# Kernel optimization log

Hardware: AMD Instinct MI355X
Metric: run time of the kernel (lower is better)

## Reference

```python
import jax, jax.numpy as jnp
import numpy as np

N = 3072      # nodes
D = 256       # embed_dim
H = 8         # heads
E = 98304     # edges (avg degree 32)
B = 16        # graphs in batch


def setup_inputs() -> dict:
    key = jax.random.key(0)
    ks = jax.random.split(key, 14)
    w = lambda k, sh: jax.random.normal(k, sh, jnp.float32) * 0.02
    return {
        "x": jax.random.normal(ks[0], (N, D), jnp.float32),
        "edge_attr": jax.random.normal(ks[1], (E, 4), jnp.float32),
        "Wq": w(ks[2], (D, D)), "bq": jnp.zeros((D,), jnp.float32),
        "Wk": w(ks[3], (D, D)), "bk": jnp.zeros((D,), jnp.float32),
        "Wv": w(ks[4], (D, D)), "bv": jnp.zeros((D,), jnp.float32),
        "Wo": w(ks[5], (D, D)), "bo": jnp.zeros((D,), jnp.float32),
        "We": w(ks[6], (4, H)), "be": jnp.zeros((H,), jnp.float32),
        "edge_index": jax.random.randint(ks[7], (2, E), 0, N),
        "batch": jnp.sort(jax.random.randint(ks[8], (N,), 0, B)),
    }


def reference(x, edge_attr, Wq, bq, Wk, bk, Wv, bv, Wo, bo, We, be,
              edge_index, batch):
    n, d = x.shape
    h = be.shape[0]
    hd = d // h
    # projections -> [h, n, hd]
    Q = (x @ Wq + bq).reshape(n, h, hd).transpose(1, 0, 2)
    K = (x @ Wk + bk).reshape(n, h, hd).transpose(1, 0, 2)
    V = (x @ Wv + bv).reshape(n, h, hd).transpose(1, 0, 2)
    # dense attention scores [h, n, n]
    scores = jnp.einsum('hnd,hmd->hnm', Q, K) / np.float32(np.sqrt(hd))
    # per-edge bias scatter-add (accumulate over duplicate edges)
    edge_bias = edge_attr @ We + be                     # [E, h]
    scores = scores.at[:, edge_index[0], edge_index[1]].add(edge_bias.T)
    # block-diagonal batch mask
    same_graph = batch[:, None] == batch[None, :]       # [n, n]
    scores = jnp.where(same_graph[None], scores, -jnp.inf)
    attn = jax.nn.softmax(scores, axis=-1)              # dropout: eval mode (identity)
    out = jnp.einsum('hnm,hmd->hnd', attn, V)           # [h, n, hd]
    out = out.transpose(1, 0, 2).reshape(n, d)
    return out @ Wo + bo
```

## Files before the change

### kernel.cpp

```cpp
#include <hip/hip_runtime.h>
#include <hip/hip_bf16.h>
#include <math.h>

#define N_NODES 3072
#define DIM     256
#define NH      8
#define HD      32
#define E_EDGES 98304
#define B_GRAPHS 16
#define MAXC    390
#define PADP    392
#define TR      16
#define SCALE   0.17677669529663689f

typedef __attribute__((ext_vector_type(8))) short bf16x8;
typedef __attribute__((ext_vector_type(4))) float f32x4;
typedef __attribute__((ext_vector_type(4))) unsigned short ushort4v;

__device__ inline unsigned short f2b(float f) {
    __hip_bfloat16 h = __float2bfloat16(f);
    return *reinterpret_cast<unsigned short*>(&h);
}
__device__ inline float b2f(unsigned short u) {
    __hip_bfloat16 h = *reinterpret_cast<__hip_bfloat16*>(&u);
    return __bfloat162float(h);
}

__global__ __launch_bounds__(256) void prep(
    const float* __restrict__ x,
    const float* __restrict__ Wq, const float* __restrict__ Wk,
    const float* __restrict__ Wv, const float* __restrict__ Wo,
    unsigned short* __restrict__ xh, unsigned short* __restrict__ xl,
    unsigned short* __restrict__ Wth, unsigned short* __restrict__ Wtl,
    const int* __restrict__ batch, int* __restrict__ counts, int* __restrict__ gstart)
{
    const int b = blockIdx.x, t = threadIdx.x;
    if (b < 768) {
        const int gid = b * 256 + t;
        float4 v = ((const float4*)x)[gid];
        ushort4v h, l;
        float c[4] = {v.x, v.y, v.z, v.w};
        #pragma unroll
        for (int i = 0; i < 4; ++i) {
            unsigned short hi = f2b(c[i]);
            h[i] = hi;
            l[i] = f2b(c[i] - b2f(hi));
        }
        ((ushort4v*)xh)[gid] = h;
        ((ushort4v*)xl)[gid] = l;
    } else if (b < 1024) {
        __shared__ float tile[32][33];
        const int wb = b - 768;
        const int mat = wb >> 6, tidx = wb & 63;
        const int tk = (tidx >> 3) * 32, tn = (tidx & 7) * 32;
        const float* W = (mat == 0) ? Wq : (mat == 1) ? Wk : (mat == 2) ? Wv : Wo;
        const int kk = t >> 5, nn = t & 31;
        #pragma unroll
        for (int p = 0; p < 4; ++p)
            tile[nn][kk + p * 8] = W[(size_t)(tk + kk + p * 8) * DIM + tn + nn];
        __syncthreads();
        const int n = t >> 3, kq = (t & 7) * 4;
        ushort4v h, l;
        #pragma unroll
        for (int i = 0; i < 4; ++i) {
            float v = tile[n][kq + i];
            unsigned short hi = f2b(v);
            h[i] = hi;
            l[i] = f2b(v - b2f(hi));
        }
        size_t o = (size_t)mat * DIM * DIM + (size_t)(tn + n) * DIM + tk + kq;
        *(ushort4v*)(Wth + o) = h;
        *(ushort4v*)(Wtl + o) = l;
    } else {
        const int i = (b - 1024) * 256 + t;
        if (i < 2 * N_NODES) counts[i] = 0;
        if (i < N_NODES) {
            int bb = batch[i];
            int bp = (i == 0) ? -1 : batch[i - 1];
            for (int g = bp + 1; g <= bb; ++g) gstart[g] = i;
            if (i == N_NODES - 1)
                for (int g = bb + 1; g <= B_GRAPHS; ++g) gstart[g] = N_NODES;
        }
    }
}

__global__ __launch_bounds__(256) void qkv_mfma(
    const unsigned short* __restrict__ xh, const unsigned short* __restrict__ xl,
    const unsigned short* __restrict__ Wth, const unsigned short* __restrict__ Wtl,
    const float* __restrict__ bq, const float* __restrict__ bk, const float* __restrict__ bv,
    unsigned short* __restrict__ Qb, unsigned short* __restrict__ Kb,
    unsigned short* __restrict__ Vb)
{
    const int t = threadIdx.x, w = t >> 6, lane = t & 63;
    const int l16 = lane & 15, lq = lane >> 4;
    const int mat = blockIdx.y >> 1;
    const int rb = blockIdx.x * 32 + (w & 1) * 16;
    const int nb = (blockIdx.y & 1) * 128 + (w >> 1) * 64;
    const unsigned short* Wh = Wth + (size_t)mat * DIM * DIM;
    const unsigned short* Wl = Wtl + (size_t)mat * DIM * DIM;

    f32x4 acc[4] = {{0,0,0,0},{0,0,0,0},{0,0,0,0},{0,0,0,0}};
    const size_t arow = (size_t)(rb + l16) * DIM + (lq << 3);

    #pragma unroll
    for (int kc = 0; kc < 8; ++kc) {
        const int k = kc * 32;
        bf16x8 ah = *(const bf16x8*)(xh + arow + k);
        bf16x8 al = *(const bf16x8*)(xl + arow + k);
        #pragma unroll
        for (int ct = 0; ct < 4; ++ct) {
            const size_t bo_ = (size_t)(nb + ct * 16 + l16) * DIM + k + (lq << 3);
            bf16x8 bh = *(const bf16x8*)(Wh + bo_);
            bf16x8 bl = *(const bf16x8*)(Wl + bo_);
            acc[ct] = __builtin_amdgcn_mfma_f32_16x16x32_bf16(ah, bh, acc[ct], 0, 0, 0);
            acc[ct] = __builtin_amdgcn_mfma_f32_16x16x32_bf16(ah, bl, acc[ct], 0, 0, 0);
            acc[ct] = __builtin_amdgcn_mfma_f32_16x16x32_bf16(al, bh, acc[ct], 0, 0, 0);
        }
    }

    const float* bias = (mat == 0) ? bq : (mat == 1) ? bk : bv;
    unsigned short* outp = (mat == 0) ? Qb : (mat == 1) ? Kb : Vb;
    #pragma unroll
    for (int ct = 0; ct < 4; ++ct) {
        const int n = nb + ct * 16 + l16;
        const float bvl = bias[n];
        #pragma unroll
        for (int r = 0; r < 4; ++r) {
            const int row = rb + lq * 4 + r;
            outp[(size_t)row * DIM + n] = f2b(acc[ct][r] + bvl);
        }
    }
}

__global__ void edge_count(const int* __restrict__ erow, int* __restrict__ counts) {
    int e = blockIdx.x * blockDim.x + threadIdx.x;
    if (e < E_EDGES) atomicAdd(&counts[erow[e]], 1);
}

__global__ __launch_bounds__(1024) void scan_rows(const int* __restrict__ counts,
                                                  int* __restrict__ rowstart) {
    __shared__ int lds[1024];
    const int t = threadIdx.x;
    int c0 = counts[3 * t], c1 = counts[3 * t + 1], c2 = counts[3 * t + 2];
    int local = c0 + c1 + c2;
    lds[t] = local;
    __syncthreads();
    for (int off = 1; off < 1024; off <<= 1) {
        int v = (t >= off) ? lds[t - off] : 0;
        __syncthreads();
        lds[t] += v;
        __syncthreads();
    }
    int incl = lds[t];
    int base = incl - local;
    rowstart[3 * t]     = base;
    rowstart[3 * t + 1] = base + c0;
    rowstart[3 * t + 2] = base + c0 + c1;
    if (t == 1023) rowstart[N_NODES] = incl;
}

__global__ void edge_fill(const int* __restrict__ erow, const int* __restrict__ ecolin,
                          const float* __restrict__ ea, const float* __restrict__ We,
                          const float* __restrict__ be,
                          const int* __restrict__ rowstart, int* __restrict__ cursor,
                          int* __restrict__ ecol, float* __restrict__ ebias) {
    int e = blockIdx.x * blockDim.x + threadIdx.x;
    if (e >= E_EDGES) return;
    int row = erow[e];
    int pos = rowstart[row] + atomicAdd(&cursor[row], 1);
    ecol[pos] = ecolin[e];
    float a0 = ea[e * 4 + 0], a1 = ea[e * 4 + 1], a2 = ea[e * 4 + 2], a3 = ea[e * 4 + 3];
    #pragma unroll
    for (int h = 0; h < NH; ++h) {
        float b = fmaf(a0, We[0 * NH + h],
                  fmaf(a1, We[1 * NH + h],
                  fmaf(a2, We[2 * NH + h],
                  fmaf(a3, We[3 * NH + h], be[h]))));
        ebias[(size_t)h * E_EDGES + pos] = b;
    }
}

__global__ __launch_bounds__(256) void attn(
    const unsigned short* __restrict__ Qb, const unsigned short* __restrict__ Kb,
    const unsigned short* __restrict__ Vb,
    const int* __restrict__ gstart, const int* __restrict__ rowstart,
    const int* __restrict__ ecol, const float* __restrict__ ebias,
    unsigned short* __restrict__ preh, unsigned short* __restrict__ prel)
{
    __shared__ float s[TR][MAXC];
    __shared__ unsigned short pb[TR][PADP];
    __shared__ float rowinv[TR];
    __shared__ int   rs_sh[TR + 1];

    const int g = blockIdx.x, tile = blockIdx.y, h = blockIdx.z;
    const int gs = gstart[g], ge = gstart[g + 1];
    const int row0 = gs + tile * TR;
    if (row0 >= ge) return;
    const int nrows = min(TR, ge - row0);
    const int ncols = ge - gs;
    const int cpad  = (ncols + 31) & ~31;
    const int t = threadIdx.x;
    const int wave = t >> 6, lane = t & 63;
    const int l16 = lane & 15, lq = lane >> 4;

    if (t <= nrows) rs_sh[t] = rowstart[row0 + t];

    {
        int arow = min(row0 + l16, N_NODES - 1);
        const bf16x8 aq = *(const bf16x8*)(Qb + (size_t)arow * DIM + h * HD + (lq << 3));
        const int nchunk16 = (ncols + 15) >> 4;
        for (int j = wave; j < nchunk16; j += 4) {
            const int c0 = j << 4;
            int krow = min(gs + c0 + l16, N_NODES - 1);
            bf16x8 bk = *(const bf16x8*)(Kb + (size_t)krow * DIM + h * HD + (lq << 3));
            f32x4 d = {0.f, 0.f, 0.f, 0.f};
            d = __builtin_amdgcn_mfma_f32_16x16x32_bf16(aq, bk, d, 0, 0, 0);
            const int col = c0 + l16, rbase = lq * 4;
            #pragma unroll
            for (int r = 0; r < 4; ++r) s[rbase + r][col] = d[r] * SCALE;
        }
    }
    __syncthreads();

    {
        int e0 = rs_sh[0], e1 = rs_sh[nrows];
        for (int idx = e0 + t; idx < e1; idx += 256) {
            int lo = 0, hi = nrows;
            while (hi - lo > 1) {
                int mid = (lo + hi) >> 1;
                if (rs_sh[mid] <= idx) lo = mid; else hi = mid;
            }
            int col = ecol[idx] - gs;
            if (col >= 0 && col < ncols)
                atomicAdd(&s[lo][col], ebias[(size_t)h * E_EDGES + idx]);
        }
    }
    __syncthreads();

    {
        const int r = t >> 4, sub = t & 15;
        if (r < nrows) {
            float m = -INFINITY;
            for (int c = sub; c < ncols; c += 16) m = fmaxf(m, s[r][c]);
            m = fmaxf(m, __shfl_xor(m, 1, 16));
            m = fmaxf(m, __shfl_xor(m, 2, 16));
            m = fmaxf(m, __shfl_xor(m, 4, 16));
            m = fmaxf(m, __shfl_xor(m, 8, 16));
            float sum = 0.f;
            for (int c = sub; c < cpad; c += 16) {
                if (c < ncols) {
                    float e = __expf(s[r][c] - m);
                    sum += e;
                    pb[r][c] = f2b(e);
                } else {
                    pb[r][c] = 0;
                }
            }
            sum += __shfl_xor(sum, 1, 16);
            sum += __shfl_xor(sum, 2, 16);
            sum += __shfl_xor(sum, 4, 16);
            sum += __shfl_xor(sum, 8, 16);
            if (sub == 0) rowinv[r] = 1.0f / sum;
        } else {
            for (int c = sub; c < cpad; c += 16) pb[r][c] = 0;
        }
    }
    __syncthreads();

    f32x4 o = {0.f, 0.f, 0.f, 0.f};
    {
        const int half = wave >> 1, par = wave & 1;
        const int kout = l16 + (half << 4);
        const int nchunk32 = cpad >> 5;
        for (int j = par; j < nchunk32; j += 2) {
            const int c0 = j << 5;
            bf16x8 ap = *(const bf16x8*)(&pb[l16][c0 + (lq << 3)]);
            bf16x8 bv;
            const int cb = c0 + (lq << 3);
            #pragma unroll
            for (int jj = 0; jj < 8; ++jj) {
                int vr = min(gs + cb + jj, N_NODES - 1);
                bv[jj] = (short)Vb[(size_t)vr * DIM + h * HD + kout];
            }
            o = __builtin_amdgcn_mfma_f32_16x16x32_bf16(ap, bv, o, 0, 0, 0);
        }
    }
    __syncthreads();
    {
        float* red = &s[0][0];
        const int rbase = lq * 4;
        #pragma unroll
        for (int r = 0; r < 4; ++r)
            red[((wave << 4) + rbase + r) * 17 + l16] = o[r];
    }
    __syncthreads();
    {
        const int row = t >> 4, kl = t & 15;
        if (row < nrows) {
            float* red = &s[0][0];
            float v0 = red[(row) * 17 + kl]        + red[(16 + row) * 17 + kl];
            float v1 = red[(32 + row) * 17 + kl]   + red[(48 + row) * 17 + kl];
            float sc = rowinv[row];
            size_t ob = (size_t)(row0 + row) * DIM + h * HD;
            float f0 = v0 * sc, f1 = v1 * sc;
            unsigned short h0 = f2b(f0), h1 = f2b(f1);
            preh[ob + kl]      = h0;
            preh[ob + 16 + kl] = h1;
            prel[ob + kl]      = f2b(f0 - b2f(h0));
            prel[ob + 16 + kl] = f2b(f1 - b2f(h1));
        }
    }
}

__global__ __launch_bounds__(256) void out_mfma(
    const unsigned short* __restrict__ preh, const unsigned short* __restrict__ prel,
    const unsigned short* __restrict__ Wth, const unsigned short* __restrict__ Wtl,
    const float* __restrict__ bo, float* __restrict__ out)
{
    const int t = threadIdx.x, w = t >> 6, lane = t & 63;
    const int l16 = lane & 15, lq = lane >> 4;
    const int rb = blockIdx.x * 16;
    const int nb = blockIdx.y * 128 + w * 32;
    const unsigned short* Wh = Wth + (size_t)3 * DIM * DIM;
    const unsigned short* Wl = Wtl + (size_t)3 * DIM * DIM;

    f32x4 acc[2] = {{0,0,0,0},{0,0,0,0}};
    const size_t arow = (size_t)(rb + l16) * DIM + (lq << 3);

    #pragma unroll
    for (int kc = 0; kc < 8; ++kc) {
        const int k = kc * 32;
        bf16x8 ah = *(const bf16x8*)(preh + arow + k);
        bf16x8 al = *(const bf16x8*)(prel + arow + k);
        #pragma unroll
        for (int ct = 0; ct < 2; ++ct) {
            const size_t bo_ = (size_t)(nb + ct * 16 + l16) * DIM + k + (lq << 3);
            bf16x8 bh = *(const bf16x8*)(Wh + bo_);
            bf16x8 bl = *(const bf16x8*)(Wl + bo_);
            acc[ct] = __builtin_amdgcn_mfma_f32_16x16x32_bf16(ah, bh, acc[ct], 0, 0, 0);
            acc[ct] = __builtin_amdgcn_mfma_f32_16x16x32_bf16(ah, bl, acc[ct], 0, 0, 0);
            acc[ct] = __builtin_amdgcn_mfma_f32_16x16x32_bf16(al, bh, acc[ct], 0, 0, 0);
        }
    }

    #pragma unroll
    for (int ct = 0; ct < 2; ++ct) {
        const int n = nb + ct * 16 + l16;
        const float bvl = bo[n];
        #pragma unroll
        for (int r = 0; r < 4; ++r) {
            const int row = rb + lq * 4 + r;
            out[(size_t)row * DIM + n] = acc[ct][r] + bvl;
        }
    }
}

extern "C" void kernel_launch(void* const* d_in, const int* in_sizes, int n_in,
                              void* d_out, int out_size, void* d_ws, size_t ws_size,
                              hipStream_t stream) {
    const float* x   = (const float*)d_in[0];
    const float* ea  = (const float*)d_in[1];
    const float* Wq  = (const float*)d_in[2];  const float* bq = (const float*)d_in[3];
    const float* Wk  = (const float*)d_in[4];  const float* bk = (const float*)d_in[5];
    const float* Wv  = (const float*)d_in[6];  const float* bv = (const float*)d_in[7];
    const float* Wo  = (const float*)d_in[8];  const float* bo = (const float*)d_in[9];
    const float* We  = (const float*)d_in[10]; const float* be = (const float*)d_in[11];
    const int*   eidx  = (const int*)d_in[12];
    const int*   batch = (const int*)d_in[13];
    const int* erow   = eidx;
    const int* ecolin = eidx + E_EDGES;

    const size_t ND = (size_t)N_NODES * DIM;
    const size_t WD = (size_t)DIM * DIM;

    unsigned short* Qb   = (unsigned short*)d_ws;
    unsigned short* Kb   = Qb + ND;
    unsigned short* Vb   = Kb + ND;
    unsigned short* preh = Vb + ND;
    unsigned short* prel = preh + ND;
    unsigned short* xh   = prel + ND;
    unsigned short* xl   = xh + ND;
    unsigned short* Wth  = xl + ND;
    unsigned short* Wtl  = Wth + 4 * WD;
    int* counts   = (int*)(Wtl + 4 * WD);
    int* cursor   = counts + N_NODES;
    int* rowstart = cursor + N_NODES;
    int* gstart   = rowstart + (N_NODES + 1);
    int* ecol     = gstart + (B_GRAPHS + 1);
    float* ebias  = (float*)(ecol + E_EDGES);

    prep<<<dim3(1048), dim3(256), 0, stream>>>(x, Wq, Wk, Wv, Wo, xh, xl, Wth, Wtl,
                                               batch, counts, gstart);
    qkv_mfma<<<dim3(96, 6), dim3(256), 0, stream>>>(xh, xl, Wth, Wtl, bq, bk, bv,
                                                    Qb, Kb, Vb);
    edge_count<<<dim3(E_EDGES / 256), dim3(256), 0, stream>>>(erow, counts);
    scan_rows<<<dim3(1), dim3(1024), 0, stream>>>(counts, rowstart);
    edge_fill<<<dim3(E_EDGES / 256), dim3(256), 0, stream>>>(erow, ecolin, ea, We, be,
                                                             rowstart, cursor, ecol, ebias);
    attn<<<dim3(B_GRAPHS, 24, NH), dim3(256), 0, stream>>>(Qb, Kb, Vb, gstart, rowstart,
                                                           ecol, ebias, preh, prel);
    out_mfma<<<dim3(192, 2), dim3(256), 0, stream>>>(preh, prel, Wth, Wtl, bo, (float*)d_out);
}
```

Measured before the change: 175.7 us.

## Fuse edge prep into prep kernel, merge scan with QKV, store V transposed

Moves edge counting and edge-bias computation into the prep kernel and merges the row scan into the QKV GEMM launch (block 0 does the scan), cutting the launch count from seven kernels to five. V is now written transposed with padded rows, so the attention PV step loads one contiguous bf16x8 vector instead of eight strided scalar gathers. Column tiles are aligned to 16, which needs a larger MAXC. Edges are packed as (edge id<<12 | col), so the bias is read indirectly through the original edge index. Risks are the extra LDS from the larger shared tile, a serial scan block sitting inside the GEMM grid, and scattered bias reads.

```diff
diff --git a/kernel.cpp b/kernel.cpp
--- a/kernel.cpp
+++ b/kernel.cpp
@@ -3,13 +3,14 @@
 #include <math.h>
 
 #define N_NODES 3072
+#define NPAD    3104
 #define DIM     256
 #define NH      8
 #define HD      32
 #define E_EDGES 98304
 #define B_GRAPHS 16
-#define MAXC    390
-#define PADP    392
+#define MAXC    422
+#define PADP    424
 #define TR      16
 #define SCALE   0.17677669529663689f
 
@@ -30,8 +31,11 @@
     const float* __restrict__ x,
     const float* __restrict__ Wq, const float* __restrict__ Wk,
     const float* __restrict__ Wv, const float* __restrict__ Wo,
+    const float* __restrict__ ea, const float* __restrict__ We,
+    const float* __restrict__ be, const int* __restrict__ erow,
     unsigned short* __restrict__ xh, unsigned short* __restrict__ xl,
     unsigned short* __restrict__ Wth, unsigned short* __restrict__ Wtl,
+    unsigned short* __restrict__ VT, float* __restrict__ ebias,
     const int* __restrict__ batch, int* __restrict__ counts, int* __restrict__ gstart)
 {
     const int b = blockIdx.x, t = threadIdx.x;
@@ -71,9 +75,9 @@
         size_t o = (size_t)mat * DIM * DIM + (size_t)(tn + n) * DIM + tk + kq;
         *(ushort4v*)(Wth + o) = h;
         *(ushort4v*)(Wtl + o) = l;
-    } else {
+    } else if (b < 1056) {
         const int i = (b - 1024) * 256 + t;
-        if (i < 2 * N_NODES) counts[i] = 0;
+        VT[(size_t)(i >> 5) * NPAD + N_NODES + (i & 31)] = 0;
         if (i < N_NODES) {
             int bb = batch[i];
             int bp = (i == 0) ? -1 : batch[i - 1];
@@ -81,110 +85,132 @@
             if (i == N_NODES - 1)
                 for (int g = bb + 1; g <= B_GRAPHS; ++g) gstart[g] = N_NODES;
         }
-    }
-}
-
-__global__ __launch_bounds__(256) void qkv_mfma(
+    } else {
+        const int e = (b - 1056) * 256 + t;
+        atomicAdd(&counts[erow[e]], 1);
+        float4 a = ((const float4*)ea)[e];
+        #pragma unroll
+        for (int h = 0; h < NH; ++h) {
+            float bb = fmaf(a.x, We[0 * NH + h],
+                       fmaf(a.y, We[1 * NH + h],
+                       fmaf(a.z, We[2 * NH + h],
+                       fmaf(a.w, We[3 * NH + h], be[h]))));
+            ebias[(size_t)h * E_EDGES + e] = bb;
+        }
+    }
+}
+
+__global__ __launch_bounds__(512) void scan_qkv(
+    const int* __restrict__ counts, int* __restrict__ rowstart,
     const unsigned short* __restrict__ xh, const unsigned short* __restrict__ xl,
     const unsigned short* __restrict__ Wth, const unsigned short* __restrict__ Wtl,
     const float* __restrict__ bq, const float* __restrict__ bk, const float* __restrict__ bv,
     unsigned short* __restrict__ Qb, unsigned short* __restrict__ Kb,
-    unsigned short* __restrict__ Vb)
+    unsigned short* __restrict__ VT)
 {
-    const int t = threadIdx.x, w = t >> 6, lane = t & 63;
+    __shared__ int slds[512];
+    if (blockIdx.x == 0) {
+        const int t = threadIdx.x;
+        int c[6], local = 0;
+        #pragma unroll
+        for (int j = 0; j < 6; ++j) { c[j] = counts[6 * t + j]; local += c[j]; }
+        slds[t] = local;
+        __syncthreads();
+        for (int off = 1; off < 512; off <<= 1) {
+            int v = (t >= off) ? slds[t - off] : 0;
+            __syncthreads();
+            slds[t] += v;
+            __syncthreads();
+        }
+        int run = slds[t] - local;
+        #pragma unroll
+        for (int j = 0; j < 6; ++j) { rowstart[6 * t + j] = run; run += c[j]; }
+        if (t == 511) rowstart[N_NODES] = run;
+        return;
+    }
+    const int u = (blockIdx.x - 1) * 2 + (threadIdx.x >> 8);
+    const int t = threadIdx.x & 255;
+    const int w = t >> 6, lane = t & 63;
     const int l16 = lane & 15, lq = lane >> 4;
-    const int mat = blockIdx.y >> 1;
-    const int rb = blockIdx.x * 32 + (w & 1) * 16;
-    const int nb = (blockIdx.y & 1) * 128 + (w >> 1) * 64;
+    const int bx = u % 96, by = u / 96;
+    const int mat = by >> 1;
+    const int rb = bx * 32 + (w & 1) * 16;
+    const int nb = (by & 1) * 128 + (w >> 1) * 64;
     const unsigned short* Wh = Wth + (size_t)mat * DIM * DIM;
     const unsigned short* Wl = Wtl + (size_t)mat * DIM * DIM;
 
     f32x4 acc[4] = {{0,0,0,0},{0,0,0,0},{0,0,0,0},{0,0,0,0}};
-    const size_t arow = (size_t)(rb + l16) * DIM + (lq << 3);
-
-    #pragma unroll
-    for (int kc = 0; kc < 8; ++kc) {
-        const int k = kc * 32;
-        bf16x8 ah = *(const bf16x8*)(xh + arow + k);
-        bf16x8 al = *(const bf16x8*)(xl + arow + k);
+
+    if (mat < 2) {
+        const size_t arow = (size_t)(rb + l16) * DIM + (lq << 3);
+        #pragma unroll
+        for (int kc = 0; kc < 8; ++kc) {
+            const int k = kc * 32;
+            bf16x8 ah = *(const bf16x8*)(xh + arow + k);
+            bf16x8 al = *(const bf16x8*)(xl + arow + k);
+            #pragma unroll
+            for (int ct = 0; ct < 4; ++ct) {
+                const size_t bo_ = (size_t)(nb + ct * 16 + l16) * DIM + k + (lq << 3);
+                bf16x8 bh = *(const bf16x8*)(Wh + bo_);
+                bf16x8 bl = *(const bf16x8*)(Wl + bo_);
+                acc[ct] = __builtin_amdgcn_mfma_f32_16x16x32_bf16(ah, bh, acc[ct], 0, 0, 0);
+                acc[ct] = __builtin_amdgcn_mfma_f32_16x16x32_bf16(ah, bl, acc[ct], 0, 0, 0);
+                acc[ct] = __builtin_amdgcn_mfma_f32_16x16x32_bf16(al, bh, acc[ct], 0, 0, 0);
+            }
+        }
+        const float* bias = (mat == 0) ? bq : bk;
+        unsigned short* outp = (mat == 0) ? Qb : Kb;
         #pragma unroll
         for (int ct = 0; ct < 4; ++ct) {
-            const size_t bo_ = (size_t)(nb + ct * 16 + l16) * DIM + k + (lq << 3);
-            bf16x8 bh = *(const bf16x8*)(Wh + bo_);
-            bf16x8 bl = *(const bf16x8*)(Wl + bo_);
-            acc[ct] = __builtin_amdgcn_mfma_f32_16x16x32_bf16(ah, bh, acc[ct], 0, 0, 0);
-            acc[ct] = __builtin_amdgcn_mfma_f32_16x16x32_bf16(ah, bl, acc[ct], 0, 0, 0);
-            acc[ct] = __builtin_amdgcn_mfma_f32_16x16x32_bf16(al, bh, acc[ct], 0, 0, 0);
-        }
-    }
-
-    const float* bias = (mat == 0) ? bq : (mat == 1) ? bk : bv;
-    unsigned short* outp = (mat == 0) ? Qb : (mat == 1) ? Kb : Vb;
-    #pragma unroll
-    for (int ct = 0; ct < 4; ++ct) {
-        const int n = nb + ct * 16 + l16;
-        const float bvl = bias[n];
-        #pragma unroll
-        for (int r = 0; r < 4; ++r) {
-            const int row = rb + lq * 4 + r;
-            outp[(size_t)row * DIM + n] = f2b(acc[ct][r] + bvl);
-        }
-    }
-}
-
-__global__ void edge_count(const int* __restrict__ erow, int* __restrict__ counts) {
-    int e = blockIdx.x * blockDim.x + threadIdx.x;
-    if (e < E_EDGES) atomicAdd(&counts[erow[e]], 1);
-}
-
-__global__ __launch_bounds__(1024) void scan_rows(const int* __restrict__ counts,
-                                                  int* __restrict__ rowstart) {
-    __shared__ int lds[1024];
-    const int t = threadIdx.x;
-    int c0 = counts[3 * t], c1 = counts[3 * t + 1], c2 = counts[3 * t + 2];
-    int local = c0 + c1 + c2;
-    lds[t] = local;
-    __syncthreads();
-    for (int off = 1; off < 1024; off <<= 1) {
-        int v = (t >= off) ? lds[t - off] : 0;
-        __syncthreads();
-        lds[t] += v;
-        __syncthreads();
-    }
-    int incl = lds[t];
-    int base = incl - local;
-    rowstart[3 * t]     = base;
-    rowstart[3 * t + 1] = base + c0;
-    rowstart[3 * t + 2] = base + c0 + c1;
-    if (t == 1023) rowstart[N_NODES] = incl;
+            const int n = nb + ct * 16 + l16;
+            const float bvl = bias[n];
+            #pragma unroll
+            for (int r = 0; r < 4; ++r)
+                outp[(size_t)(rb + lq * 4 + r) * DIM + n] = f2b(acc[ct][r] + bvl);
+        }
+    } else {
+        const size_t brow = (size_t)(rb + l16) * DIM + (lq << 3);
+        #pragma unroll
+        for (int kc = 0; kc < 8; ++kc) {
+            const int k = kc * 32;
+            bf16x8 bxh = *(const bf16x8*)(xh + brow + k);
+            bf16x8 bxl = *(const bf16x8*)(xl + brow + k);
+            #pragma unroll
+            for (int ct = 0; ct < 4; ++ct) {
+                const size_t ao_ = (size_t)(nb + ct * 16 + l16) * DIM + k + (lq << 3);
+                bf16x8 awh = *(const bf16x8*)(Wh + ao_);
+                bf16x8 awl = *(const bf16x8*)(Wl + ao_);
+                acc[ct] = __builtin_amdgcn_mfma_f32_16x16x32_bf16(awh, bxh, acc[ct], 0, 0, 0);
+                acc[ct] = __builtin_amdgcn_mfma_f32_16x16x32_bf16(awh, bxl, acc[ct], 0, 0, 0);
+                acc[ct] = __builtin_amdgcn_mfma_f32_16x16x32_bf16(awl, bxh, acc[ct], 0, 0, 0);
+            }
+        }
+        #pragma unroll
+        for (int ct = 0; ct < 4; ++ct) {
+            #pragma unroll
+            for (int r = 0; r < 4; ++r) {
+                const int ncol = nb + ct * 16 + lq * 4 + r;
+                VT[(size_t)ncol * NPAD + rb + l16] = f2b(acc[ct][r] + bv[ncol]);
+            }
+        }
+    }
 }
 
 __global__ void edge_fill(const int* __restrict__ erow, const int* __restrict__ ecolin,
-                          const float* __restrict__ ea, const float* __restrict__ We,
-                          const float* __restrict__ be,
                           const int* __restrict__ rowstart, int* __restrict__ cursor,
-                          int* __restrict__ ecol, float* __restrict__ ebias) {
+                          unsigned int* __restrict__ epack) {
     int e = blockIdx.x * blockDim.x + threadIdx.x;
     if (e >= E_EDGES) return;
     int row = erow[e];
     int pos = rowstart[row] + atomicAdd(&cursor[row], 1);
-    ecol[pos] = ecolin[e];
-    float a0 = ea[e * 4 + 0], a1 = ea[e * 4 + 1], a2 = ea[e * 4 + 2], a3 = ea[e * 4 + 3];
-    #pragma unroll
-    for (int h = 0; h < NH; ++h) {
-        float b = fmaf(a0, We[0 * NH + h],
-                  fmaf(a1, We[1 * NH + h],
-                  fmaf(a2, We[2 * NH + h],
-                  fmaf(a3, We[3 * NH + h], be[h]))));
-        ebias[(size_t)h * E_EDGES + pos] = b;
-    }
+    epack[pos] = ((unsigned int)e << 12) | (unsigned int)ecolin[e];
 }
 
 __global__ __launch_bounds__(256) void attn(
     const unsigned short* __restrict__ Qb, const unsigned short* __restrict__ Kb,
-    const unsigned short* __restrict__ Vb,
+    const unsigned short* __restrict__ VT,
     const int* __restrict__ gstart, const int* __restrict__ rowstart,
-    const int* __restrict__ ecol, const float* __restrict__ ebias,
+    const unsigned int* __restrict__ epack, const float* __restrict__ ebias,
     unsigned short* __restrict__ preh, unsigned short* __restrict__ prel)
 {
     __shared__ float s[TR][MAXC];
@@ -198,7 +224,10 @@
     if (row0 >= ge) return;
     const int nrows = min(TR, ge - row0);
     const int ncols = ge - gs;
-    const int cpad  = (ncols + 31) & ~31;
+    const int ags   = gs & ~15;
+    const int coff  = gs - ags;
+    const int tcols = coff + ncols;
+    const int cpad  = (tcols + 31) & ~31;
     const int t = threadIdx.x;
     const int wave = t >> 6, lane = t & 63;
     const int l16 = lane & 15, lq = lane >> 4;
@@ -208,10 +237,10 @@
     {
         int arow = min(row0 + l16, N_NODES - 1);
         const bf16x8 aq = *(const bf16x8*)(Qb + (size_t)arow * DIM + h * HD + (lq << 3));
-        const int nchunk16 = (ncols + 15) >> 4;
+        const int nchunk16 = (tcols + 15) >> 4;
         for (int j = wave; j < nchunk16; j += 4) {
             const int c0 = j << 4;
-            int krow = min(gs + c0 + l16, N_NODES - 1);
+            int krow = min(ags + c0 + l16, N_NODES - 1);
             bf16x8 bk = *(const bf16x8*)(Kb + (size_t)krow * DIM + h * HD + (lq << 3));
             f32x4 d = {0.f, 0.f, 0.f, 0.f};
             d = __builtin_amdgcn_mfma_f32_16x16x32_bf16(aq, bk, d, 0, 0, 0);
@@ -225,14 +254,15 @@
     {
         int e0 = rs_sh[0], e1 = rs_sh[nrows];
         for (int idx = e0 + t; idx < e1; idx += 256) {
+            unsigned int p = epack[idx];
+            int col = (int)(p & 0xFFFu) - gs;
             int lo = 0, hi = nrows;
             while (hi - lo > 1) {
                 int mid = (lo + hi) >> 1;
                 if (rs_sh[mid] <= idx) lo = mid; else hi = mid;
             }
-            int col = ecol[idx] - gs;
             if (col >= 0 && col < ncols)
-                atomicAdd(&s[lo][col], ebias[(size_t)h * E_EDGES + idx]);
+                atomicAdd(&s[lo][coff + col], ebias[(size_t)h * E_EDGES + (p >> 12)]);
         }
     }
     __syncthreads();
@@ -241,14 +271,14 @@
         const int r = t >> 4, sub = t & 15;
         if (r < nrows) {
             float m = -INFINITY;
-            for (int c = sub; c < ncols; c += 16) m = fmaxf(m, s[r][c]);
+            for (int c = coff + sub; c < tcols; c += 16) m = fmaxf(m, s[r][c]);
             m = fmaxf(m, __shfl_xor(m, 1, 16));
             m = fmaxf(m, __shfl_xor(m, 2, 16));
             m = fmaxf(m, __shfl_xor(m, 4, 16));
             m = fmaxf(m, __shfl_xor(m, 8, 16));
             float sum = 0.f;
             for (int c = sub; c < cpad; c += 16) {
-                if (c < ncols) {
+                if (c >= coff && c < tcols) {
                     float e = __expf(s[r][c] - m);
                     sum += e;
                     pb[r][c] = f2b(e);
@@ -272,16 +302,11 @@
         const int half = wave >> 1, par = wave & 1;
         const int kout = l16 + (half << 4);
         const int nchunk32 = cpad >> 5;
+        const unsigned short* vrow = VT + (size_t)(h * HD + kout) * NPAD + ags + (lq << 3);
         for (int j = par; j < nchunk32; j += 2) {
             const int c0 = j << 5;
             bf16x8 ap = *(const bf16x8*)(&pb[l16][c0 + (lq << 3)]);
-            bf16x8 bv;
-            const int cb = c0 + (lq << 3);
-            #pragma unroll
-            for (int jj = 0; jj < 8; ++jj) {
-                int vr = min(gs + cb + jj, N_NODES - 1);
-                bv[jj] = (short)Vb[(size_t)vr * DIM + h * HD + kout];
-            }
+            bf16x8 bv = *(const bf16x8*)(vrow + c0);
             o = __builtin_amdgcn_mfma_f32_16x16x32_bf16(ap, bv, o, 0, 0, 0);
         }
     }
@@ -348,10 +373,8 @@
         const int n = nb + ct * 16 + l16;
         const float bvl = bo[n];
         #pragma unroll
-        for (int r = 0; r < 4; ++r) {
-            const int row = rb + lq * 4 + r;
-            out[(size_t)row * DIM + n] = acc[ct][r] + bvl;
-        }
+        for (int r = 0; r < 4; ++r)
+            out[(size_t)(rb + lq * 4 + r) * DIM + n] = acc[ct][r] + bvl;
     }
 }
 
@@ -375,8 +398,8 @@
 
     unsigned short* Qb   = (unsigned short*)d_ws;
     unsigned short* Kb   = Qb + ND;
-    unsigned short* Vb   = Kb + ND;
-    unsigned short* preh = Vb + ND;
+    unsigned short* VT   = Kb + ND;
+    unsigned short* preh = VT + (size_t)DIM * NPAD;
     unsigned short* prel = preh + ND;
     unsigned short* xh   = prel + ND;
     unsigned short* xl   = xh + ND;
@@ -386,18 +409,18 @@
     int* cursor   = counts + N_NODES;
     int* rowstart = cursor + N_NODES;
     int* gstart   = rowstart + (N_NODES + 1);
-    int* ecol     = gstart + (B_GRAPHS + 1);
-    float* ebias  = (float*)(ecol + E_EDGES);
-
-    prep<<<dim3(1048), dim3(256), 0, stream>>>(x, Wq, Wk, Wv, Wo, xh, xl, Wth, Wtl,
+    unsigned int* epack = (unsigned int*)(gstart + (B_GRAPHS + 1));
+    float* ebias  = (float*)(epack + E_EDGES);
+
+    hipMemsetAsync(counts, 0, 2 * N_NODES * sizeof(int), stream);
+    prep<<<dim3(1440), dim3(256), 0, stream>>>(x, Wq, Wk, Wv, Wo, ea, We, be, erow,
+                                               xh, xl, Wth, Wtl, VT, ebias,
                                                batch, counts, gstart);
-    qkv_mfma<<<dim3(96, 6), dim3(256), 0, stream>>>(xh, xl, Wth, Wtl, bq, bk, bv,
-                                                    Qb, Kb, Vb);
-    edge_count<<<dim3(E_EDGES / 256), dim3(256), 0, stream>>>(erow, counts);
-    scan_rows<<<dim3(1), dim3(1024), 0, stream>>>(counts, rowstart);
-    edge_fill<<<dim3(E_EDGES / 256), dim3(256), 0, stream>>>(erow, ecolin, ea, We, be,
-                                                             rowstart, cursor, ecol, ebias);
-    attn<<<dim3(B_GRAPHS, 24, NH), dim3(256), 0, stream>>>(Qb, Kb, Vb, gstart, rowstart,
-                                                           ecol, ebias, preh, prel);
+    scan_qkv<<<dim3(289), dim3(512), 0, stream>>>(counts, rowstart, xh, xl, Wth, Wtl,
+                                                  bq, bk, bv, Qb, Kb, VT);
+    edge_fill<<<dim3(E_EDGES / 256), dim3(256), 0, stream>>>(erow, ecolin, rowstart,
+                                                             cursor, epack);
+    attn<<<dim3(B_GRAPHS, 24, NH), dim3(256), 0, stream>>>(Qb, Kb, VT, gstart, rowstart,
+                                                           epack, ebias, preh, prel);
     out_mfma<<<dim3(192, 2), dim3(256), 0, stream>>>(preh, prel, Wth, Wtl, bo, (float*)d_out);
 }
```

Result: no change. 178.1 us (+1.4%).
